# Performance work log

Hardware: AMD Instinct MI355X
Metric: run time of the kernel (lower is better)

Reference implementation:

```python
import jax, jax.numpy as jnp
import numpy as np

B, S, D = 4, 4096, 256


def setup_inputs() -> dict:
    key = jax.random.key(0)
    ks = jax.random.split(key, 7)
    s = 1.0 / np.sqrt(D)
    return {
        "x": jax.random.normal(ks[0], (B, S, D), dtype=jnp.float32),
        "Wq": jax.random.uniform(ks[1], (D, D), jnp.float32, -s, s),
        "bq": jax.random.uniform(ks[2], (D,), jnp.float32, -s, s),
        "Wk": jax.random.uniform(ks[3], (D, D), jnp.float32, -s, s),
        "bk": jax.random.uniform(ks[4], (D,), jnp.float32, -s, s),
        "Wv": jax.random.uniform(ks[5], (D, D), jnp.float32, -s, s),
        "bv": jax.random.uniform(ks[6], (D,), jnp.float32, -s, s),
    }


def reference(x, Wq, bq, Wk, bk, Wv, bv):
    # nn.Linear: y = x @ W.T + b
    Q = jnp.einsum("bsd,ed->bse", x, Wq) + bq
    K = jnp.einsum("bsd,ed->bse", x, Wk) + bk
    V = jnp.einsum("bsd,ed->bse", x, Wv) + bv
    dk = Q.shape[-1]
    scores = jnp.einsum("bqd,bkd->bqk", Q, K) / jnp.sqrt(jnp.float32(dk))
    # NOTE: original applies softmax over dim=1 (the query axis), not -1.
    attn = jax.nn.softmax(scores, axis=1)
    out = jnp.einsum("bqk,bkd->bqd", attn, V)
    return out
```

## Files before the change

kernel.cpp:

```cpp
#include <hip/hip_runtime.h>

typedef short bf16x8 __attribute__((ext_vector_type(8)));
typedef float f32x4 __attribute__((ext_vector_type(4)));
typedef unsigned short u16;

#define S_LEN 4096
#define D_DIM 256
#define NROW  16384

__device__ __forceinline__ u16 f2bf(float f) {
    union { float f; unsigned u; } v; v.f = f;
    unsigned r = v.u + 0x7FFFu + ((v.u >> 16) & 1u);
    return (u16)(r >> 16);
}
__device__ __forceinline__ float bf2f(u16 h) {
    union { unsigned u; float f; } v; v.u = ((unsigned)h) << 16; return v.f;
}

__device__ __forceinline__ size_t fr_qk(int t, int kk) {
    return (size_t)t * 4096 + kk * 512;
}
__device__ __forceinline__ size_t fr_v(int p, int dt, int kk2) {
    return (size_t)p * 16384 + (dt * 2 + kk2) * 512;
}
__device__ __forceinline__ size_t e_base(int b, int kc, int qt) {
    return ((size_t)(b * 32768 + kc * 256 + qt)) * 512;
}

__device__ __forceinline__ void gll16(const u16* g, u16* l) {
    __builtin_amdgcn_global_load_lds(
        (const __attribute__((address_space(1))) unsigned int*)g,
        (__attribute__((address_space(3))) unsigned int*)l, 16, 0, 0);
}

#define WAITV4 asm volatile("s_waitcnt vmcnt(4)" ::: "memory")
#define WAITV2 asm volatile("s_waitcnt vmcnt(2)" ::: "memory")
#define WAITV0 asm volatile("s_waitcnt vmcnt(0)" ::: "memory")
#define WAITLGKM0 asm volatile("s_waitcnt lgkmcnt(0)" ::: "memory")
#define MEMFENCE asm volatile("" ::: "memory")

__global__ __launch_bounds__(256) void wconv(
    const float* __restrict__ Wq, const float* __restrict__ Wk,
    const float* __restrict__ Wv, u16* __restrict__ Wf)
{
    int i = blockIdx.x * 256 + threadIdx.x;
    int m = i >> 13;
    int idx = i & 8191;
    int ocol = idx >> 5;
    int d0 = (idx & 31) * 8;
    const float* s = (m == 0 ? Wq : (m == 1 ? Wk : Wv)) + ocol * 256 + d0;
    float4 v0 = *reinterpret_cast<const float4*>(s);
    float4 v1 = *reinterpret_cast<const float4*>(s + 4);
    union { ushort4 h[2]; int4 q; } t;
    t.h[0] = make_ushort4(f2bf(v0.x), f2bf(v0.y), f2bf(v0.z), f2bf(v0.w));
    t.h[1] = make_ushort4(f2bf(v1.x), f2bf(v1.y), f2bf(v1.z), f2bf(v1.w));
    size_t off = (size_t)m * 65536 + fr_qk(ocol >> 4, d0 >> 5)
               + ((d0 >> 3) & 3) * 128 + (ocol & 15) * 8;
    *reinterpret_cast<int4*>(Wf + off) = t.q;
}

__global__ __launch_bounds__(256) void qkv_proj(
    const float* __restrict__ x, const u16* __restrict__ Wf,
    const float* __restrict__ bq, const float* __restrict__ bk,
    const float* __restrict__ bv,
    u16* __restrict__ Qf, u16* __restrict__ Kf, u16* __restrict__ Vf)
{
    __shared__ u16 xs[32][264];
    const int tid = threadIdx.x;
    const int r0 = blockIdx.x * 32;

    #pragma unroll
    for (int i = 0; i < 8; ++i) {
        int c = i * 256 + tid;
        int row = c >> 6, c4 = c & 63;
        float4 v = reinterpret_cast<const float4*>(x + (size_t)(r0 + row) * D_DIM)[c4];
        *reinterpret_cast<ushort4*>(&xs[row][c4 * 4]) =
            make_ushort4(f2bf(v.x), f2bf(v.y), f2bf(v.z), f2bf(v.w));
    }
    __syncthreads();

    const int w = tid >> 6, l = tid & 63, lr = l & 15, lg = l >> 4;
    const int c0 = w * 64;

    bf16x8 a[2][8];
    #pragma unroll
    for (int qs = 0; qs < 2; ++qs)
        #pragma unroll
        for (int kk = 0; kk < 8; ++kk)
            a[qs][kk] = *reinterpret_cast<const bf16x8*>(&xs[qs * 16 + lr][kk * 32 + lg * 8]);

    const float* Bs[3] = {bq, bk, bv};

    #pragma unroll
    for (int m = 0; m < 3; ++m) {
        const u16* Wm = Wf + (size_t)m * 65536;
        f32x4 acc[2][4] = {};
        #pragma unroll
        for (int kk = 0; kk < 8; ++kk) {
            #pragma unroll
            for (int cf = 0; cf < 4; ++cf) {
                bf16x8 wfr = *reinterpret_cast<const bf16x8*>(
                    Wm + fr_qk(w * 4 + cf, kk) + l * 8);
                acc[0][cf] = __builtin_amdgcn_mfma_f32_16x16x32_bf16(a[0][kk], wfr, acc[0][cf], 0, 0, 0);
                acc[1][cf] = __builtin_amdgcn_mfma_f32_16x16x32_bf16(a[1][kk], wfr, acc[1][cf], 0, 0, 0);
            }
        }
        if (m < 2) {
            u16* outp = (m == 0) ? Qf : Kf;
            int t = r0 >> 4;
            #pragma unroll
            for (int qs = 0; qs < 2; ++qs) {
                #pragma unroll
                for (int cf = 0; cf < 4; ++cf) {
                    int col = c0 + cf * 16 + lr;
                    float bias = Bs[m][col];
                    size_t base = fr_qk(t + qs, col >> 5) + ((col >> 3) & 3) * 128 + (col & 7);
                    #pragma unroll
                    for (int r = 0; r < 4; ++r)
                        outp[base + (lg * 4 + r) * 8] = f2bf(acc[qs][cf][r] + bias);
                }
            }
        } else {
            int p  = (r0 >> 12) * 64 + ((r0 & 4095) >> 6);
            int kb = r0 & 63;
            #pragma unroll
            for (int qs = 0; qs < 2; ++qs) {
                #pragma unroll
                for (int cf = 0; cf < 4; ++cf) {
                    int d = c0 + cf * 16 + lr;
                    float bias = bv[d];
                    #pragma unroll
                    for (int r = 0; r < 4; ++r) {
                        int key = kb + qs * 16 + lg * 4 + r;
                        size_t off = fr_v(p, d >> 4, key >> 5)
                                   + ((key >> 3) & 3) * 128 + (d & 15) * 8 + (key & 7);
                        Vf[off] = f2bf(acc[qs][cf][r] + bias);
                    }
                }
            }
        }
    }
}

__global__ __launch_bounds__(256, 4) void score_exp(
    const u16* __restrict__ Qf, const u16* __restrict__ Kf,
    u16* __restrict__ Ef, float* __restrict__ Zp, int write_e)
{
    __shared__ __align__(16) u16 Qls[2][8192];
    const int tid = threadIdx.x, blk = blockIdx.x;
    const int xcd = blk & 7, sub = blk >> 3;
    const int b  = xcd >> 1;
    const int qe = ((xcd & 1) << 2) | (sub & 3);
    const int ktile = sub >> 2;
    const int w = tid >> 6, l = tid & 63, lr = l & 15, lg = l >> 4;
    const int k0 = ktile * 128;

    bf16x8 kreg[2][8];
    #pragma unroll
    for (int ks = 0; ks < 2; ++ks) {
        const int tk = b * 256 + (k0 >> 4) + w * 2 + ks;
        #pragma unroll
        for (int kk = 0; kk < 8; ++kk)
            kreg[ks][kk] = *reinterpret_cast<const bf16x8*>(Kf + fr_qk(tk, kk) + l * 8);
    }

    #define STAGE_Q(qt_, nb_) do { \
        const u16* g_ = Qf + ((size_t)(b * 256 + (qt_) * 2)) * 4096 + (w * 4) * 512 + l * 8; \
        u16* d_ = &Qls[nb_][(w * 4) * 512]; \
        _Pragma("unroll") \
        for (int f_ = 0; f_ < 4; ++f_) gll16(g_ + f_ * 512, d_ + f_ * 512); \
    } while (0)

    const int qt0 = qe * 16;
    STAGE_Q(qt0, 0);
    __syncthreads();

    float Z[2][4] = {};
    const float SC = 0.0625f;
    const int kc = ktile * 4 + w;

    for (int it = 0; it < 16; ++it) {
        const int cur = it & 1;
        if (it < 15) STAGE_Q(qt0 + it + 1, cur ^ 1);

        f32x4 acc[2][2] = {};
        #pragma unroll
        for (int kk = 0; kk < 8; ++kk) {
            #pragma unroll
            for (int qf = 0; qf < 2; ++qf) {
                bf16x8 qfr = *reinterpret_cast<const bf16x8*>(
                    &Qls[cur][(qf * 8 + kk) * 512 + l * 8]);
                acc[0][qf] = __builtin_amdgcn_mfma_f32_16x16x32_bf16(kreg[0][kk], qfr, acc[0][qf], 0, 0, 0);
                acc[1][qf] = __builtin_amdgcn_mfma_f32_16x16x32_bf16(kreg[1][kk], qfr, acc[1][qf], 0, 0, 0);
            }
        }
        #pragma unroll
        for (int ks = 0; ks < 2; ++ks) {
            #pragma unroll
            for (int qf = 0; qf < 2; ++qf) {
                float e0 = __expf(acc[ks][qf][0] * SC);
                float e1 = __expf(acc[ks][qf][1] * SC);
                float e2 = __expf(acc[ks][qf][2] * SC);
                float e3 = __expf(acc[ks][qf][3] * SC);
                Z[ks][0] += e0; Z[ks][1] += e1; Z[ks][2] += e2; Z[ks][3] += e3;
                if (write_e) {
                    size_t ad = e_base(b, kc, (qt0 + it) * 2 + qf)
                              + (ks * 2 + (lg >> 1)) * 128 + lr * 8 + (lg & 1) * 4;
                    *reinterpret_cast<ushort4*>(Ef + ad) =
                        make_ushort4(f2bf(e0), f2bf(e1), f2bf(e2), f2bf(e3));
                }
            }
        }
        __syncthreads();
    }

    #pragma unroll
    for (int ks = 0; ks < 2; ++ks) {
        #pragma unroll
        for (int r = 0; r < 4; ++r) {
            float z = Z[ks][r];
            z += __shfl_xor(z, 1);
            z += __shfl_xor(z, 2);
            z += __shfl_xor(z, 4);
            z += __shfl_xor(z, 8);
            if (lr == 0)
                Zp[qe * NROW + b * S_LEN + k0 + w * 32 + ks * 16 + lg * 4 + r] = z;
        }
    }
    #undef STAGE_Q
}

__global__ __launch_bounds__(256) void zrecip(
    const float* __restrict__ Zp, float* __restrict__ rZ)
{
    int i = blockIdx.x * 256 + threadIdx.x;
    float s = Zp[i];
    #pragma unroll
    for (int p = 1; p < 8; ++p) s += Zp[p * NROW + i];
    rZ[i] = 1.0f / s;
}

__global__ __launch_bounds__(256) void zlog(
    const float* __restrict__ Zp, float* __restrict__ LZ)
{
    int i = blockIdx.x * 256 + threadIdx.x;
    float s = Zp[i];
    #pragma unroll
    for (int p = 1; p < 8; ++p) s += Zp[p * NROW + i];
    LZ[i] = logf(s);
}

__global__ __launch_bounds__(256) void vscale(
    u16* __restrict__ Vf, const float* __restrict__ rZ)
{
    int i = blockIdx.x * 256 + threadIdx.x;
    int frag = i >> 6, l8 = i & 63;
    int p = frag >> 5, sub = frag & 31, kk2 = sub & 1;
    int b = p >> 6, kt = p & 63;
    int kbase = b * S_LEN + kt * 64 + kk2 * 32 + (l8 >> 4) * 8;
    float4 rz0 = *reinterpret_cast<const float4*>(&rZ[kbase]);
    float4 rz1 = *reinterpret_cast<const float4*>(&rZ[kbase + 4]);
    ushort4* vp = reinterpret_cast<ushort4*>(Vf + (size_t)i * 8);
    ushort4 a = vp[0], c = vp[1];
    vp[0] = make_ushort4(f2bf(bf2f(a.x) * rz0.x), f2bf(bf2f(a.y) * rz0.y),
                         f2bf(bf2f(a.z) * rz0.z), f2bf(bf2f(a.w) * rz0.w));
    vp[1] = make_ushort4(f2bf(bf2f(c.x) * rz1.x), f2bf(bf2f(c.y) * rz1.y),
                         f2bf(bf2f(c.z) * rz1.z), f2bf(bf2f(c.w) * rz1.w));
}

__global__ __launch_bounds__(256, 4) void pv_gemm(
    const u16* __restrict__ Ef, const u16* __restrict__ Vf, float* __restrict__ out)
{
    __shared__ __align__(16) u16 Vls[2][8192];

    const int tid = threadIdx.x, blk = blockIdx.x;
    const int xcd = blk & 7, sub = blk >> 3;
    const int b  = xcd >> 1;
    const int ks = ((xcd & 1) << 1) | (sub & 1);
    const int qt64 = sub >> 1;
    const int w = tid >> 6, l = tid & 63, lr = l & 15, lg = l >> 4;
    const int qh = w & 1, dh = w >> 1;

    #define EADDR(it_, j_) \
        (Ef + e_base(b, ks * 32 + (it_), qt64 * 4 + qh * 2 + (j_)) + l * 8)

    #define STAGE_V(it_, nb_) do { \
        const int kc_ = ks * 32 + (it_); \
        const size_t vb_ = ((size_t)(b * 64 + (kc_ >> 1))) * 16384 + (kc_ & 1) * 512; \
        _Pragma("unroll") \
        for (int f_ = 0; f_ < 4; ++f_) { \
            int dt_ = w * 4 + f_; \
            gll16(Vf + vb_ + (size_t)(dt_ * 2) * 512 + l * 8, &Vls[nb_][dt_ * 512]); \
        } \
    } while (0)

    #define COMPUTE(nb_, e0_, e1_) do { \
        __builtin_amdgcn_s_setprio(1); \
        _Pragma("unroll") \
        for (int dt = 0; dt < 8; ++dt) { \
            bf16x8 vfr = *reinterpret_cast<const bf16x8*>( \
                &Vls[nb_][(dh * 8 + dt) * 512 + l * 8]); \
            acc[0][dt] = __builtin_amdgcn_mfma_f32_16x16x32_bf16(e0_, vfr, acc[0][dt], 0, 0, 0); \
            acc[1][dt] = __builtin_amdgcn_mfma_f32_16x16x32_bf16(e1_, vfr, acc[1][dt], 0, 0, 0); \
        } \
        __builtin_amdgcn_s_setprio(0); \
    } while (0)

    #define BODY(it_, eC0_, eC1_, eN0_, eN1_) do { \
        STAGE_V((it_) + 1, ((it_) + 1) & 1); \
        MEMFENCE; \
        eN0_ = *reinterpret_cast<const bf16x8*>(EADDR((it_) + 2, 0)); \
        eN1_ = *reinterpret_cast<const bf16x8*>(EADDR((it_) + 2, 1)); \
        MEMFENCE; \
        COMPUTE((it_) & 1, eC0_, eC1_); \
        WAITV2; \
        __builtin_amdgcn_s_barrier(); \
        MEMFENCE; \
    } while (0)

    f32x4 acc[2][8] = {};
    bf16x8 eA0, eA1, eB0, eB1, eC0, eC1;

    eA0 = *reinterpret_cast<const bf16x8*>(EADDR(0, 0));
    eA1 = *reinterpret_cast<const bf16x8*>(EADDR(0, 1));
    MEMFENCE;
    STAGE_V(0, 0);
    MEMFENCE;
    eB0 = *reinterpret_cast<const bf16x8*>(EADDR(1, 0));
    eB1 = *reinterpret_cast<const bf16x8*>(EADDR(1, 1));
    MEMFENCE;
    WAITV2;
    __builtin_amdgcn_s_barrier();
    MEMFENCE;

    #pragma unroll 1
    for (int base = 0; base < 30; base += 3) {
        BODY(base,     eA0, eA1, eC0, eC1);
        BODY(base + 1, eB0, eB1, eA0, eA1);
        BODY(base + 2, eC0, eC1, eB0, eB1);
    }
    STAGE_V(31, 1);
    COMPUTE(0, eA0, eA1);
    WAITV0;
    __builtin_amdgcn_s_barrier();
    MEMFENCE;
    COMPUTE(1, eB0, eB1);

    const int qg = b * S_LEN + qt64 * 64 + qh * 32;
    const int dg = dh * 128;
    #pragma unroll
    for (int qf = 0; qf < 2; ++qf) {
        #pragma unroll
        for (int dt = 0; dt < 8; ++dt) {
            #pragma unroll
            for (int r = 0; r < 4; ++r) {
                unsafeAtomicAdd(&out[(size_t)(qg + qf * 16 + lg * 4 + r) * D_DIM
                                     + dg + dt * 16 + lr],
                                acc[qf][dt][r]);
            }
        }
    }
    #undef EADDR
    #undef STAGE_V
    #undef COMPUTE
    #undef BODY
}

__global__ __launch_bounds__(512, 1) void attn_out_fb(
    const u16* __restrict__ Qf, const u16* __restrict__ Kf, const u16* __restrict__ Vf,
    const float* __restrict__ LZ, float* __restrict__ out)
{
    __shared__ __align__(16) u16 Kls[3][8192];
    __shared__ __align__(16) u16 Vls[4][8192];
    __shared__ __align__(16) u16 ps[8][2][1280];
    __shared__ __align__(16) float lzs[1024];

    const int tid = threadIdx.x, blk = blockIdx.x;
    const int xcd = blk & 7, sub = blk >> 3;
    const int b  = xcd >> 1;
    const int kq = ((xcd & 1) << 1) | (sub & 1);
    const int qtile = sub >> 1;
    const int w = tid >> 6, l = tid & 63, lr = l & 15, lg = l >> 4;
    const int q0 = qtile * 256 + w * 32;
    const int base_tk = b * 256;
    const int kt0 = kq * 32;

    bf16x8 qreg[2][8];
    #pragma unroll
    for (int qs = 0; qs < 2; ++qs) {
        const int tq = base_tk + ((q0 + qs * 16) >> 4);
        #pragma unroll
        for (int kk = 0; kk < 8; ++kk)
            qreg[qs][kk] = *reinterpret_cast<const bf16x8*>(Qf + fr_qk(tq, kk) + l * 8);
    }

    #define STAGE(kt_) do { \
        if (w < 4) { \
            const u16* g_ = Kf + ((size_t)(base_tk + (kt0 + (kt_)) * 2)) * 4096 + (w * 4) * 512 + l * 8; \
            u16* d_ = &Kls[(kt_) % 3][(w * 4) * 512]; \
            _Pragma("unroll") \
            for (int f_ = 0; f_ < 4; ++f_) gll16(g_ + f_ * 512, d_ + f_ * 512); \
        } else { \
            const int kta_ = kt0 + (kt_); \
            const size_t vb_ = ((size_t)(b * 64 + (kta_ >> 1))) * 16384 + (kta_ & 1) * 512; \
            const int dt0_ = (w - 4) * 4; \
            _Pragma("unroll") \
            for (int f_ = 0; f_ < 4; ++f_) \
                gll16(Vf + vb_ + (size_t)(dt0_ + f_) * 1024 + l * 8, &Vls[(kt_) % 4][(dt0_ + f_) * 512]); \
        } \
    } while (0)

    #define QK(kt_) do { \
        const u16* kb_ = &Kls[(kt_) % 3][0]; \
        __builtin_amdgcn_s_setprio(1); \
        _Pragma("unroll") \
        for (int kk = 0; kk < 8; ++kk) { \
            bf16x8 k0_ = *reinterpret_cast<const bf16x8*>(kb_ + kk * 512 + l * 8); \
            bf16x8 k1_ = *reinterpret_cast<const bf16x8*>(kb_ + (8 + kk) * 512 + l * 8); \
            sacc[0][0] = __builtin_amdgcn_mfma_f32_16x16x32_bf16(qreg[0][kk], k0_, sacc[0][0], 0, 0, 0); \
            sacc[0][1] = __builtin_amdgcn_mfma_f32_16x16x32_bf16(qreg[1][kk], k0_, sacc[0][1], 0, 0, 0); \
            sacc[1][0] = __builtin_amdgcn_mfma_f32_16x16x32_bf16(qreg[0][kk], k1_, sacc[1][0], 0, 0, 0); \
            sacc[1][1] = __builtin_amdgcn_mfma_f32_16x16x32_bf16(qreg[1][kk], k1_, sacc[1][1], 0, 0, 0); \
        } \
        __builtin_amdgcn_s_setprio(0); \
    } while (0)

    #define PV(j_) do { \
        const u16* vb_ = &Vls[(j_) % 4][0]; \
        const u16* pb_ = &ps[w][(j_) & 1][0]; \
        bf16x8 af0_ = *reinterpret_cast<const bf16x8*>(pb_ + lr * 40 + lg * 8); \
        bf16x8 af1_ = *reinterpret_cast<const bf16x8*>(pb_ + (16 + lr) * 40 + lg * 8); \
        __builtin_amdgcn_s_setprio(1); \
        _Pragma("unroll") \
        for (int dt = 0; dt < 16; ++dt) { \
            bf16x8 vf_ = *reinterpret_cast<const bf16x8*>(vb_ + dt * 512 + l * 8); \
            oacc[0][dt] = __builtin_amdgcn_mfma_f32_16x16x32_bf16(af0_, vf_, oacc[0][dt], 0, 0, 0); \
            oacc[1][dt] = __builtin_amdgcn_mfma_f32_16x16x32_bf16(af1_, vf_, oacc[1][dt], 0, 0, 0); \
        } \
        __builtin_amdgcn_s_setprio(0); \
    } while (0)

    #define SM(kt_) do { \
        u16* pw_ = &ps[w][(kt_) & 1][0]; \
        _Pragma("unroll") \
        for (int cf = 0; cf < 2; ++cf) { \
            float Lv_ = lzs[(kt_) * 32 + cf * 16 + lr]; \
            _Pragma("unroll") \
            for (int qs = 0; qs < 2; ++qs) \
                _Pragma("unroll") \
                for (int r = 0; r < 4; ++r) { \
                    float p_ = __expf(fmaf(sacc[cf][qs][r], SC, -Lv_)); \
                    pw_[(qs * 16 + lg * 4 + r) * 40 + cf * 16 + lr] = f2bf(p_); \
                } \
        } \
    } while (0)

    f32x4 oacc[2][16] = {};
    const float SC = 0.0625f;

    f32x4 lzv;
    if (tid < 256)
        lzv = *reinterpret_cast<const f32x4*>(LZ + b * S_LEN + kt0 * 32 + tid * 4);
    STAGE(0);
    STAGE(1);
    if (tid < 256)
        *reinterpret_cast<f32x4*>(&lzs[tid * 4]) = lzv;
    WAITLGKM0;
    WAITV4;
    __builtin_amdgcn_s_barrier();
    MEMFENCE;

    #pragma unroll 1
    for (int kt = 0; kt < 30; ++kt) {
        STAGE(kt + 2);
        f32x4 sacc[2][2] = {};
        QK(kt);
        if (kt > 0) PV(kt - 1);
        SM(kt);
        WAITV4;
        __builtin_amdgcn_s_barrier();
        MEMFENCE;
    }
    {
        f32x4 sacc[2][2] = {};
        QK(30); PV(29); SM(30);
        WAITV0;
        __builtin_amdgcn_s_barrier();
        MEMFENCE;
    }
    {
        f32x4 sacc[2][2] = {};
        QK(31); PV(30); SM(31); PV(31);
    }

    #pragma unroll
    for (int qs = 0; qs < 2; ++qs) {
        #pragma unroll
        for (int dt = 0; dt < 16; ++dt) {
            #pragma unroll
            for (int r = 0; r < 4; ++r) {
                int row = q0 + qs * 16 + lg * 4 + r;
                unsafeAtomicAdd(&out[((size_t)(b * S_LEN + row)) * D_DIM + dt * 16 + lr],
                                oacc[qs][dt][r]);
            }
        }
    }
    #undef STAGE
    #undef QK
    #undef PV
    #undef SM
}

extern "C" void kernel_launch(void* const* d_in, const int* in_sizes, int n_in,
                              void* d_out, int out_size, void* d_ws, size_t ws_size,
                              hipStream_t stream) {
    const float* x  = (const float*)d_in[0];
    const float* Wq = (const float*)d_in[1];
    const float* bq = (const float*)d_in[2];
    const float* Wk = (const float*)d_in[3];
    const float* bk = (const float*)d_in[4];
    const float* Wv = (const float*)d_in[5];
    const float* bv = (const float*)d_in[6];
    float* out = (float*)d_out;

    u16* Qf = (u16*)d_ws;
    u16* Kf = Qf + (size_t)NROW * D_DIM;
    u16* Vf = Kf + (size_t)NROW * D_DIM;
    u16* Wf = Vf + (size_t)NROW * D_DIM;
    float* Zp = (float*)(Wf + 196608);
    float* rZ = Zp + 8 * NROW;
    u16* Ef = (u16*)(rZ + NROW);

    const size_t need = (size_t)((char*)Ef - (char*)d_ws) + (size_t)4 * 32768 * 512 * 2;

    hipMemsetAsync(out, 0, (size_t)NROW * D_DIM * sizeof(float), stream);
    wconv<<<96, 256, 0, stream>>>(Wq, Wk, Wv, Wf);
    qkv_proj<<<NROW / 32, 256, 0, stream>>>(x, Wf, bq, bk, bv, Qf, Kf, Vf);

    if (ws_size >= need) {
        score_exp<<<1024, 256, 0, stream>>>(Qf, Kf, Ef, Zp, 1);
        zrecip<<<NROW / 256, 256, 0, stream>>>(Zp, rZ);
        vscale<<<2048, 256, 0, stream>>>(Vf, rZ);
        pv_gemm<<<1024, 256, 0, stream>>>(Ef, Vf, out);
    } else {
        score_exp<<<1024, 256, 0, stream>>>(Qf, Kf, Qf , Zp, 0);
        zlog<<<NROW / 256, 256, 0, stream>>>(Zp, rZ);
        attn_out_fb<<<256, 512, 0, stream>>>(Qf, Kf, Vf, rZ, out);
    }
}
```

Measured before the change: 161.4 us.

## Load V fragments directly from global in pv_gemm, dropping LDS staging and barriers

Replaces the LDS double-buffered V staging (global_load_lds plus barriers and a triple-buffered E register pipeline) in pv_gemm with a simple loop. Each wave now loads its E and V fragments straight from global memory into registers and issues the MFMAs, with the loop unrolled by 2. Launch bounds drop from 4 to 3 blocks per SM to leave room for the extra registers. This removes barrier synchronisation and LDS traffic, but each V fragment is now fetched separately by both wave pairs that share a dh, so global/L2 traffic rises and latency hiding depends on the compiler's scheduling.

```diff
diff --git a/kernel.cpp b/kernel.cpp
--- a/kernel.cpp
+++ b/kernel.cpp
@@ -34,7 +34,6 @@
 }
 
 #define WAITV4 asm volatile("s_waitcnt vmcnt(4)" ::: "memory")
-#define WAITV2 asm volatile("s_waitcnt vmcnt(2)" ::: "memory")
 #define WAITV0 asm volatile("s_waitcnt vmcnt(0)" ::: "memory")
 #define WAITLGKM0 asm volatile("s_waitcnt lgkmcnt(0)" ::: "memory")
 #define MEMFENCE asm volatile("" ::: "memory")
@@ -268,11 +267,9 @@
                          f2bf(bf2f(c.z) * rz1.z), f2bf(bf2f(c.w) * rz1.w));
 }
 
-__global__ __launch_bounds__(256, 4) void pv_gemm(
+__global__ __launch_bounds__(256, 3) void pv_gemm(
     const u16* __restrict__ Ef, const u16* __restrict__ Vf, float* __restrict__ out)
 {
-    __shared__ __align__(16) u16 Vls[2][8192];
-
     const int tid = threadIdx.x, blk = blockIdx.x;
     const int xcd = blk & 7, sub = blk >> 3;
     const int b  = xcd >> 1;
@@ -281,70 +278,47 @@
     const int w = tid >> 6, l = tid & 63, lr = l & 15, lg = l >> 4;
     const int qh = w & 1, dh = w >> 1;
 
-    #define EADDR(it_, j_) \
-        (Ef + e_base(b, ks * 32 + (it_), qt64 * 4 + qh * 2 + (j_)) + l * 8)
-
-    #define STAGE_V(it_, nb_) do { \
-        const int kc_ = ks * 32 + (it_); \
-        const size_t vb_ = ((size_t)(b * 64 + (kc_ >> 1))) * 16384 + (kc_ & 1) * 512; \
-        _Pragma("unroll") \
-        for (int f_ = 0; f_ < 4; ++f_) { \
-            int dt_ = w * 4 + f_; \
-            gll16(Vf + vb_ + (size_t)(dt_ * 2) * 512 + l * 8, &Vls[nb_][dt_ * 512]); \
-        } \
-    } while (0)
-
-    #define COMPUTE(nb_, e0_, e1_) do { \
-        __builtin_amdgcn_s_setprio(1); \
-        _Pragma("unroll") \
-        for (int dt = 0; dt < 8; ++dt) { \
-            bf16x8 vfr = *reinterpret_cast<const bf16x8*>( \
-                &Vls[nb_][(dh * 8 + dt) * 512 + l * 8]); \
-            acc[0][dt] = __builtin_amdgcn_mfma_f32_16x16x32_bf16(e0_, vfr, acc[0][dt], 0, 0, 0); \
-            acc[1][dt] = __builtin_amdgcn_mfma_f32_16x16x32_bf16(e1_, vfr, acc[1][dt], 0, 0, 0); \
-        } \
-        __builtin_amdgcn_s_setprio(0); \
-    } while (0)
-
-    #define BODY(it_, eC0_, eC1_, eN0_, eN1_) do { \
-        STAGE_V((it_) + 1, ((it_) + 1) & 1); \
-        MEMFENCE; \
-        eN0_ = *reinterpret_cast<const bf16x8*>(EADDR((it_) + 2, 0)); \
-        eN1_ = *reinterpret_cast<const bf16x8*>(EADDR((it_) + 2, 1)); \
-        MEMFENCE; \
-        COMPUTE((it_) & 1, eC0_, eC1_); \
-        WAITV2; \
-        __builtin_amdgcn_s_barrier(); \
-        MEMFENCE; \
-    } while (0)
+    const u16* ebase = Ef + e_base(b, ks * 32, qt64 * 4 + qh * 2) + l * 8;
+    const size_t vstep = (size_t)l * 8;
 
     f32x4 acc[2][8] = {};
-    bf16x8 eA0, eA1, eB0, eB1, eC0, eC1;
-
-    eA0 = *reinterpret_cast<const bf16x8*>(EADDR(0, 0));
-    eA1 = *reinterpret_cast<const bf16x8*>(EADDR(0, 1));
-    MEMFENCE;
-    STAGE_V(0, 0);
-    MEMFENCE;
-    eB0 = *reinterpret_cast<const bf16x8*>(EADDR(1, 0));
-    eB1 = *reinterpret_cast<const bf16x8*>(EADDR(1, 1));
-    MEMFENCE;
-    WAITV2;
-    __builtin_amdgcn_s_barrier();
-    MEMFENCE;
-
-    #pragma unroll 1
-    for (int base = 0; base < 30; base += 3) {
-        BODY(base,     eA0, eA1, eC0, eC1);
-        BODY(base + 1, eB0, eB1, eA0, eA1);
-        BODY(base + 2, eC0, eC1, eB0, eB1);
-    }
-    STAGE_V(31, 1);
-    COMPUTE(0, eA0, eA1);
-    WAITV0;
-    __builtin_amdgcn_s_barrier();
-    MEMFENCE;
-    COMPUTE(1, eB0, eB1);
+
+    #pragma unroll 2
+    for (int it = 0; it < 32; ++it) {
+        const int kc = ks * 32 + it;
+        const size_t vb = ((size_t)(b * 64 + (kc >> 1))) * 16384 + (kc & 1) * 512;
+
+        bf16x8 e0 = *reinterpret_cast<const bf16x8*>(ebase + (size_t)it * 131072);
+        bf16x8 e1 = *reinterpret_cast<const bf16x8*>(ebase + (size_t)it * 131072 + 512);
+
+        bf16x8 v0 = *reinterpret_cast<const bf16x8*>(Vf + vb + (size_t)(dh * 8 + 0) * 1024 + vstep);
+        bf16x8 v1 = *reinterpret_cast<const bf16x8*>(Vf + vb + (size_t)(dh * 8 + 1) * 1024 + vstep);
+        bf16x8 v2 = *reinterpret_cast<const bf16x8*>(Vf + vb + (size_t)(dh * 8 + 2) * 1024 + vstep);
+        bf16x8 v3 = *reinterpret_cast<const bf16x8*>(Vf + vb + (size_t)(dh * 8 + 3) * 1024 + vstep);
+        bf16x8 v4 = *reinterpret_cast<const bf16x8*>(Vf + vb + (size_t)(dh * 8 + 4) * 1024 + vstep);
+        bf16x8 v5 = *reinterpret_cast<const bf16x8*>(Vf + vb + (size_t)(dh * 8 + 5) * 1024 + vstep);
+        bf16x8 v6 = *reinterpret_cast<const bf16x8*>(Vf + vb + (size_t)(dh * 8 + 6) * 1024 + vstep);
+        bf16x8 v7 = *reinterpret_cast<const bf16x8*>(Vf + vb + (size_t)(dh * 8 + 7) * 1024 + vstep);
+
+        __builtin_amdgcn_s_setprio(1);
+        acc[0][0] = __builtin_amdgcn_mfma_f32_16x16x32_bf16(e0, v0, acc[0][0], 0, 0, 0);
+        acc[1][0] = __builtin_amdgcn_mfma_f32_16x16x32_bf16(e1, v0, acc[1][0], 0, 0, 0);
+        acc[0][1] = __builtin_amdgcn_mfma_f32_16x16x32_bf16(e0, v1, acc[0][1], 0, 0, 0);
+        acc[1][1] = __builtin_amdgcn_mfma_f32_16x16x32_bf16(e1, v1, acc[1][1], 0, 0, 0);
+        acc[0][2] = __builtin_amdgcn_mfma_f32_16x16x32_bf16(e0, v2, acc[0][2], 0, 0, 0);
+        acc[1][2] = __builtin_amdgcn_mfma_f32_16x16x32_bf16(e1, v2, acc[1][2], 0, 0, 0);
+        acc[0][3] = __builtin_amdgcn_mfma_f32_16x16x32_bf16(e0, v3, acc[0][3], 0, 0, 0);
+        acc[1][3] = __builtin_amdgcn_mfma_f32_16x16x32_bf16(e1, v3, acc[1][3], 0, 0, 0);
+        acc[0][4] = __builtin_amdgcn_mfma_f32_16x16x32_bf16(e0, v4, acc[0][4], 0, 0, 0);
+        acc[1][4] = __builtin_amdgcn_mfma_f32_16x16x32_bf16(e1, v4, acc[1][4], 0, 0, 0);
+        acc[0][5] = __builtin_amdgcn_mfma_f32_16x16x32_bf16(e0, v5, acc[0][5], 0, 0, 0);
+        acc[1][5] = __builtin_amdgcn_mfma_f32_16x16x32_bf16(e1, v5, acc[1][5], 0, 0, 0);
+        acc[0][6] = __builtin_amdgcn_mfma_f32_16x16x32_bf16(e0, v6, acc[0][6], 0, 0, 0);
+        acc[1][6] = __builtin_amdgcn_mfma_f32_16x16x32_bf16(e1, v6, acc[1][6], 0, 0, 0);
+        acc[0][7] = __builtin_amdgcn_mfma_f32_16x16x32_bf16(e0, v7, acc[0][7], 0, 0, 0);
+        acc[1][7] = __builtin_amdgcn_mfma_f32_16x16x32_bf16(e1, v7, acc[1][7], 0, 0, 0);
+        __builtin_amdgcn_s_setprio(0);
+    }
 
     const int qg = b * S_LEN + qt64 * 64 + qh * 32;
     const int dg = dh * 128;
@@ -360,10 +334,6 @@
             }
         }
     }
-    #undef EADDR
-    #undef STAGE_V
-    #undef COMPUTE
-    #undef BODY
 }
 
 __global__ __launch_bounds__(512, 1) void attn_out_fb(
```

Result: slower. 171.6 us (+6.3%).
